# Kernel optimization log

Measured on AMD Instinct MI355X. Metric: run time of the kernel, lower is better.

The kernel has to match this reference:

```python
import jax, jax.numpy as jnp
import numpy as np

N = 20000   # nodes
E = 160000  # edges
C = 512     # input_size / channels
D = 16      # edge_size
H = 256     # hidden_size
EPS = 1e-5  # BatchNorm eps (eval mode, init running stats: mean=0, var=1)


def setup_inputs() -> dict:
    key = jax.random.key(0)
    ks = jax.random.split(key, 24)
    w = lambda k, shape: (jax.random.normal(k, shape, jnp.float32) * 0.02)
    inp = {
        "x": jax.random.normal(ks[0], (N, C), jnp.float32),
        "edge_index": jax.random.randint(ks[1], (2, E), 0, N, jnp.int32),
        "edge_attr": jax.random.normal(ks[2], (E, D), jnp.float32),
        "goal_feat": jax.random.normal(ks[3], (N, C), jnp.float32),
        # CGConv 1
        "Wf1": w(ks[4], (2 * C + D, C)), "bf1": jnp.zeros((C,), jnp.float32),
        "Ws1": w(ks[5], (2 * C + D, C)), "bs1": jnp.zeros((C,), jnp.float32),
        "g1": jnp.ones((C,), jnp.float32), "be1": jnp.zeros((C,), jnp.float32),
        # CGConv 2
        "Wf2": w(ks[6], (2 * C + D, C)), "bf2": jnp.zeros((C,), jnp.float32),
        "Ws2": w(ks[7], (2 * C + D, C)), "bs2": jnp.zeros((C,), jnp.float32),
        "g2": jnp.ones((C,), jnp.float32), "be2": jnp.zeros((C,), jnp.float32),
        # GCNConv 3, 4
        "W3": w(ks[8], (C, H)), "b3": jnp.zeros((H,), jnp.float32),
        "W4": w(ks[9], (H, H)), "b4": jnp.zeros((H,), jnp.float32),
        # distance MLP: Lin(H+C -> C), ReLU, Lin(C -> 1)
        "Wd1": w(ks[10], (H + C, C)), "bd1": jnp.zeros((C,), jnp.float32),
        "Wd2": w(ks[11], (C, 1)), "bd2": jnp.zeros((1,), jnp.float32),
    }
    return inp


def cg_conv(x, src, dst, edge_attr, Wf, bf, Ws, bs, gamma, beta):
    # PyG CGConv: z = x_i || x_j || e;  m = sigmoid(lin_f(z)) * softplus(lin_s(z))
    # aggr='add' at targets, BatchNorm (eval, init stats), residual.
    z = jnp.concatenate([x[dst], x[src], edge_attr], axis=-1)  # [E, 2C+D]
    m = jax.nn.sigmoid(z @ Wf + bf) * jax.nn.softplus(z @ Ws + bs)  # [E, C]
    agg = jax.ops.segment_sum(m, dst, num_segments=N)  # [N, C]
    agg = agg * (gamma / jnp.sqrt(1.0 + EPS)) + beta   # BN eval (mean=0, var=1)
    return agg + x


def gcn_conv(x, src, dst, W, b):
    # PyG GCNConv with add_self_loops=True, normalize=True
    h = x @ W  # [N, out]
    loop = jnp.arange(N, dtype=src.dtype)
    s = jnp.concatenate([src, loop])
    d = jnp.concatenate([dst, loop])
    deg = jax.ops.segment_sum(jnp.ones_like(d, jnp.float32), d, num_segments=N)
    dinv = jnp.where(deg > 0, jax.lax.rsqrt(jnp.maximum(deg, 1.0)), 0.0)
    norm = dinv[s] * dinv[d]  # [E+N]
    out = jax.ops.segment_sum(norm[:, None] * h[s], d, num_segments=N)
    return out + b


def reference(x, edge_index, edge_attr, goal_feat,
              Wf1, bf1, Ws1, bs1, g1, be1,
              Wf2, bf2, Ws2, bs2, g2, be2,
              W3, b3, W4, b4, Wd1, bd1, Wd2, bd2):
    src = edge_index[0]  # x_j (source)
    dst = edge_index[1]  # x_i (target)
    h = jax.nn.relu(cg_conv(x, src, dst, edge_attr, Wf1, bf1, Ws1, bs1, g1, be1))
    h = jax.nn.relu(cg_conv(h, src, dst, edge_attr, Wf2, bf2, Ws2, bs2, g2, be2))
    h = jax.nn.relu(gcn_conv(h, src, dst, W3, b3))
    h = jax.nn.relu(gcn_conv(h, src, dst, W4, b4))
    z = jnp.concatenate([h, goal_feat], axis=1)  # [N, H+C]
    pred_dist = jax.nn.relu(z @ Wd1 + bd1) @ Wd2 + bd2  # [N, 1]
    return pred_dist, h
```

## Files before the change

kernel.cpp:

```cpp
#include <hip/hip_runtime.h>
#include <stdint.h>

#define NNODES 20000
#define NEDGES 160000
#define NPAD   20096

typedef float f32x4 __attribute__((ext_vector_type(4)));
typedef float f32x2 __attribute__((ext_vector_type(2)));
typedef short s16x8 __attribute__((ext_vector_type(8)));
typedef unsigned int u32x4 __attribute__((ext_vector_type(4)));
typedef _Float16 h16x2 __attribute__((ext_vector_type(2)));

__device__ __forceinline__ float b2f(unsigned short b) {
    unsigned int u = ((unsigned int)b) << 16;
    return __builtin_bit_cast(float, u);
}
__device__ __forceinline__ unsigned short f2b(float f) {
    unsigned int u = __builtin_bit_cast(unsigned int, f);
    unsigned int r = (u + 0x7FFFu + ((u >> 16) & 1u)) >> 16;
    return (unsigned short)r;
}
__device__ __forceinline__ f32x2 unpack2(unsigned int u) {
    f32x2 r;
    r.x = __builtin_bit_cast(float, u << 16);
    r.y = __builtin_bit_cast(float, u & 0xFFFF0000u);
    return r;
}
__device__ __forceinline__ unsigned int packh2(float a, float b) {
    h16x2 h = { (_Float16)a, (_Float16)b };
    return __builtin_bit_cast(unsigned int, h);
}
__device__ __forceinline__ float dot2h(unsigned int a, unsigned int b, float c) {
#if __has_builtin(__builtin_amdgcn_fdot2)
    return __builtin_amdgcn_fdot2(__builtin_bit_cast(h16x2, a),
                                  __builtin_bit_cast(h16x2, b), c, false);
#else
    float d;
    asm("v_dot2_f32_f16 %0, %1, %2, %3" : "=v"(d) : "v"(a), "v"(b), "v"(c));
    return d;
#endif
}

__global__ __launch_bounds__(256) void gemm_bt_kernel(
    const unsigned short* __restrict__ A,
    const unsigned short* __restrict__ BT,
    float* __restrict__ Cf,
    unsigned short* __restrict__ Cb,
    int M, int N, int K,
    const float* __restrict__ bias)
{
    __shared__ unsigned short As[128 * 32];
    __shared__ unsigned short Bs[128 * 32];
    const int tid  = threadIdx.x;
    const int wid  = tid >> 6;
    const int lane = tid & 63;
    const int bm = blockIdx.x * 128;
    const int bn = blockIdx.y * 128;
    const int wm = (wid & 1) * 64;
    const int wn = (wid >> 1) * 64;

    f32x4 acc[4][4];
#pragma unroll
    for (int i = 0; i < 4; i++)
#pragma unroll
        for (int j = 0; j < 4; j++) acc[i][j] = {0.f, 0.f, 0.f, 0.f};

    for (int k0 = 0; k0 < K; k0 += 32) {
#pragma unroll
        for (int r = 0; r < 2; r++) {
            int flat = r * 256 + tid;
            int row  = flat >> 2;
            int part = flat & 3;
            const unsigned short* ga = A  + (size_t)(bm + row) * K + k0 + part * 8;
            const unsigned short* gb = BT + (size_t)(bn + row) * K + k0 + part * 8;
            __builtin_amdgcn_global_load_lds(
                (const __attribute__((address_space(1))) unsigned int*)ga,
                (__attribute__((address_space(3))) unsigned int*)&As[flat * 8], 16, 0, 0);
            __builtin_amdgcn_global_load_lds(
                (const __attribute__((address_space(1))) unsigned int*)gb,
                (__attribute__((address_space(3))) unsigned int*)&Bs[flat * 8], 16, 0, 0);
        }
        __syncthreads();

        const int kq = (lane >> 4) * 8;
        const int rl = lane & 15;
        s16x8 af[4], bfr[4];
#pragma unroll
        for (int mi = 0; mi < 4; mi++)
            af[mi] = *(const s16x8*)&As[(wm + mi * 16 + rl) * 32 + kq];
#pragma unroll
        for (int ni = 0; ni < 4; ni++)
            bfr[ni] = *(const s16x8*)&Bs[(wn + ni * 16 + rl) * 32 + kq];
#pragma unroll
        for (int mi = 0; mi < 4; mi++)
#pragma unroll
            for (int ni = 0; ni < 4; ni++)
                acc[mi][ni] = __builtin_amdgcn_mfma_f32_16x16x32_bf16(
                    af[mi], bfr[ni], acc[mi][ni], 0, 0, 0);
        __syncthreads();
    }

    const int cl = lane & 15;
    const int rq = (lane >> 4) * 4;
#pragma unroll
    for (int mi = 0; mi < 4; mi++)
#pragma unroll
        for (int ni = 0; ni < 4; ni++)
#pragma unroll
            for (int r = 0; r < 4; r++) {
                int row = bm + wm + mi * 16 + rq + r;
                int col = bn + wn + ni * 16 + cl;
                float v = acc[mi][ni][r];
                if (Cb) {
                    if (bias) v = fmaxf(v + bias[col], 0.f);
                    Cb[(size_t)row * N + col] = f2b(v);
                } else {
                    Cf[(size_t)row * N + col] = v;
                }
            }
}

__global__ void count_kernel(const int* __restrict__ ei, int* __restrict__ counts) {
    int e = blockIdx.x * blockDim.x + threadIdx.x;
    if (e < NEDGES) atomicAdd(&counts[ei[NEDGES + e]], 1);
}

__global__ __launch_bounds__(1024) void scan_kernel(const int* __restrict__ counts,
                                                    int* __restrict__ row_ptr)
{
    __shared__ int sdata[1024];
    const int t = threadIdx.x;
    int vals[20];
    const int base = t * 20;
    int lsum = 0;
#pragma unroll
    for (int j = 0; j < 20; j++) {
        int idx = base + j;
        int v = (idx < NNODES) ? counts[idx] : 0;
        vals[j] = v; lsum += v;
    }
    sdata[t] = lsum;
    __syncthreads();
    for (int off = 1; off < 1024; off <<= 1) {
        int v = (t >= off) ? sdata[t - off] : 0;
        __syncthreads();
        sdata[t] += v;
        __syncthreads();
    }
    int run = sdata[t] - lsum;
#pragma unroll
    for (int j = 0; j < 20; j++) {
        int idx = base + j;
        if (idx < NNODES) row_ptr[idx] = run;
        run += vals[j];
    }
    if (t == 1023) row_ptr[NNODES] = sdata[1023];
}

__global__ void fill_kernel(const int* __restrict__ ei,
                            const int* __restrict__ row_ptr,
                            int* __restrict__ cursor,
                            int2* __restrict__ csr)
{
    int e = blockIdx.x * blockDim.x + threadIdx.x;
    if (e >= NEDGES) return;
    int dst = ei[NEDGES + e];
    int p = row_ptr[dst] + atomicAdd(&cursor[dst], 1);
    csr[p] = make_int2(ei[e], e);
}

__global__ void dinv_kernel(const int* __restrict__ row_ptr, float* __restrict__ dinv) {
    int i = blockIdx.x * blockDim.x + threadIdx.x;
    if (i < NNODES) {
        int deg = row_ptr[i + 1] - row_ptr[i] + 1;
        dinv[i] = rsqrtf((float)deg);
    }
}

__global__ void pad_copy_kernel(const float* __restrict__ src,
                                unsigned short* __restrict__ dst,
                                int valid_rows, int cols, long total)
{
    long idx = (long)blockIdx.x * blockDim.x + threadIdx.x;
    if (idx >= total) return;
    int n = (int)(idx / cols);
    dst[idx] = (n < valid_rows) ? f2b(src[idx]) : (unsigned short)0;
}

__global__ void pack_cgw_kernel(const float* __restrict__ Wf,
                                const float* __restrict__ Ws,
                                unsigned short* __restrict__ out)
{
    int idx = blockIdx.x * blockDim.x + threadIdx.x;
    if (idx >= 2048 * 512) return;
    int j = idx >> 9;
    int k = idx & 511;
    int half = (j >= 1024);
    int jj = j & 1023;
    int c  = (jj >> 2) * 2 + (jj & 1);
    int fs = (jj >> 1) & 1;
    const float* W = fs ? Ws : Wf;
    float v = W[(size_t)(half ? 512 + k : k) * 512 + c];
    out[idx] = f2b(v);
}

__global__ void pack_t_kernel(const float* __restrict__ W,
                              unsigned short* __restrict__ WT,
                              int K, int Nout)
{
    long idx = (long)blockIdx.x * blockDim.x + threadIdx.x;
    if (idx >= (long)K * Nout) return;
    int j = (int)(idx / K);
    int k = (int)(idx % K);
    WT[idx] = f2b(W[(size_t)k * Nout + j]);
}

__global__ void pack_we_kernel(const float* __restrict__ Wf,
                               const float* __restrict__ Ws,
                               unsigned int* __restrict__ out)
{
    int idx = blockIdx.x * blockDim.x + threadIdx.x;
    if (idx >= 8192) return;
    int q  = idx & 3;
    int c2 = (idx >> 2) & 255;
    int k  = idx >> 10;
    const float* W = (q >> 1) ? Ws : Wf;
    int c = c2 * 2 + (q & 1);
    float v0 = W[(size_t)(1024 + 2 * k) * 512 + c];
    float v1 = W[(size_t)(1024 + 2 * k + 1) * 512 + c];
    out[idx] = packh2(v0, v1);
}

__global__ void pack_ea_kernel(const int2* __restrict__ csr,
                               const float* __restrict__ ea,
                               unsigned int* __restrict__ out)
{
    int idx = blockIdx.x * blockDim.x + threadIdx.x;
    if (idx >= NEDGES * 8) return;
    int i = idx >> 3;
    int j = idx & 7;
    int eid = csr[i].y;
    out[idx] = packh2(ea[(size_t)eid * 16 + 2 * j], ea[(size_t)eid * 16 + 2 * j + 1]);
}

#define CG_NPB 4
__global__ __launch_bounds__(256, 1) void cg_gather_kernel(
    const unsigned short* __restrict__ P,
    const int* __restrict__ row_ptr,
    const int2* __restrict__ csr,
    const u32x4* __restrict__ wE,
    const u32x4* __restrict__ eapk,
    const float* __restrict__ bfv,
    const float* __restrict__ bsv,
    const float* __restrict__ g,
    const float* __restrict__ be,
    const float* __restrict__ xresf,
    const unsigned short* __restrict__ xresb,
    unsigned short* __restrict__ hout)
{
    const int tid = threadIdx.x;
    const int c0  = tid * 2;
    const int nbase = blockIdx.x * CG_NPB;

    u32x4 w[8];
#pragma unroll
    for (int k = 0; k < 8; k++) w[k] = wE[k * 256 + tid];

    const f32x2 bfx = *(const f32x2*)&bfv[c0];
    const f32x2 bsx = *(const f32x2*)&bsv[c0];
    const f32x2 gv  = *(const f32x2*)&g[c0];
    const f32x2 bev = *(const f32x2*)&be[c0];
    const float rs = rsqrtf(1.f + 1e-5f);

    for (int n = nbase; n < nbase + CG_NPB; n++) {
        if (n >= NNODES) {
            *(unsigned int*)&hout[(size_t)n * 512 + c0] = 0;
            continue;
        }
        const unsigned short* Pd = P + (size_t)n * 2048;
        const uint2 qb = *(const uint2*)(Pd + c0 * 2);
        const f32x2 baseF = unpack2(qb.x) + bfx;
        const f32x2 baseS = unpack2(qb.y) + bsx;

        f32x2 acc = {0.f, 0.f};
        const int i0 = row_ptr[n], i1 = row_ptr[n + 1];

        auto do_edge = [&](int i) {
            const int sx = __builtin_amdgcn_readfirstlane(csr[i].x);
            u32x4 a0 = eapk[(size_t)i * 2];
            u32x4 a1 = eapk[(size_t)i * 2 + 1];
            uint2 q = *(const uint2*)(P + (size_t)sx * 2048 + 1024 + c0 * 2);
            float f0 = baseF.x, f1 = baseF.y, s0 = baseS.x, s1 = baseS.y;
#pragma unroll
            for (int k = 0; k < 4; k++) {
                f0 = dot2h(a0[k], w[k][0], f0);
                f1 = dot2h(a0[k], w[k][1], f1);
                s0 = dot2h(a0[k], w[k][2], s0);
                s1 = dot2h(a0[k], w[k][3], s1);
            }
#pragma unroll
            for (int k = 0; k < 4; k++) {
                f0 = dot2h(a1[k], w[4 + k][0], f0);
                f1 = dot2h(a1[k], w[4 + k][1], f1);
                s0 = dot2h(a1[k], w[4 + k][2], s0);
                s1 = dot2h(a1[k], w[4 + k][3], s1);
            }
            f32x2 pf = unpack2(q.x);
            f32x2 ps = unpack2(q.y);
            f0 += pf.x; f1 += pf.y; s0 += ps.x; s1 += ps.y;
            float sp0 = __logf(1.f + __expf(s0));
            float sp1 = __logf(1.f + __expf(s1));
            float sg0 = __builtin_amdgcn_rcpf(1.f + __expf(-f0));
            float sg1 = __builtin_amdgcn_rcpf(1.f + __expf(-f1));
            acc.x = fmaf(sp0, sg0, acc.x);
            acc.y = fmaf(sp1, sg1, acc.y);
        };

        int i = i0;
        for (; i + 1 < i1; i += 2) {
            do_edge(i);
            do_edge(i + 1);
        }
        if (i < i1) do_edge(i);

        f32x2 res;
        if (xresf) {
            res = *(const f32x2*)&xresf[(size_t)n * 512 + c0];
        } else {
            res = unpack2(*(const unsigned int*)&xresb[(size_t)n * 512 + c0]);
        }
        float v0 = fmaxf(acc.x * (gv.x * rs) + bev.x + res.x, 0.f);
        float v1 = fmaxf(acc.y * (gv.y * rs) + bev.y + res.y, 0.f);
        unsigned int packed = (unsigned int)f2b(v0) | ((unsigned int)f2b(v1) << 16);
        *(unsigned int*)&hout[(size_t)n * 512 + c0] = packed;
    }
}

__global__ __launch_bounds__(256) void gcn_gather_kernel(
    const unsigned short* __restrict__ pre,
    const int* __restrict__ row_ptr,
    const int2* __restrict__ csr,
    const float* __restrict__ dinv,
    const float* __restrict__ b,
    unsigned short* __restrict__ hout,
    float* __restrict__ doutf)
{
    const int tid = threadIdx.x;
    const int n = blockIdx.x * 2 + (tid >> 7);
    const int c = (tid & 127) * 2;
    if (n >= NNODES) {
        if (n < NPAD) *(unsigned int*)&hout[(size_t)n * 256 + c] = 0;
        return;
    }
    const float din = dinv[n];
    f32x2 acc = {0.f, 0.f};
    const int i0 = row_ptr[n], i1 = row_ptr[n + 1];
    if (i0 < i1) {
        int sx = __builtin_amdgcn_readfirstlane(csr[i0].x);
        float dv = dinv[sx];
        unsigned int pv = *(const unsigned int*)&pre[(size_t)sx * 256 + c];
        for (int i = i0; i < i1; i++) {
            float cdv = dv; unsigned int cpv = pv;
            if (i + 1 < i1) {
                int sx2 = __builtin_amdgcn_readfirstlane(csr[i + 1].x);
                dv = dinv[sx2];
                pv = *(const unsigned int*)&pre[(size_t)sx2 * 256 + c];
            }
            f32x2 p = unpack2(cpv);
            acc.x = fmaf(cdv, p.x, acc.x);
            acc.y = fmaf(cdv, p.y, acc.y);
        }
    }
    f32x2 self = unpack2(*(const unsigned int*)&pre[(size_t)n * 256 + c]);
    const f32x2 bv = *(const f32x2*)&b[c];
    float v0 = fmaxf(fmaf(acc.x, din, din * din * self.x) + bv.x, 0.f);
    float v1 = fmaxf(fmaf(acc.y, din, din * din * self.y) + bv.y, 0.f);
    *(unsigned int*)&hout[(size_t)n * 256 + c] =
        (unsigned int)f2b(v0) | ((unsigned int)f2b(v1) << 16);
    if (doutf) {
        f32x2 vv = {v0, v1};
        *(f32x2*)&doutf[(size_t)n * 256 + c] = vv;
    }
}

__global__ void build_zc_kernel(const unsigned short* __restrict__ h4,
                                const float* __restrict__ goal,
                                unsigned short* __restrict__ zc)
{
    long idx = (long)blockIdx.x * blockDim.x + threadIdx.x;
    if (idx >= (long)NPAD * 768) return;
    int n = (int)(idx / 768);
    int c = (int)(idx % 768);
    unsigned short v = 0;
    if (n < NNODES)
        v = (c < 256) ? h4[(size_t)n * 256 + c]
                      : f2b(goal[(size_t)n * 512 + (c - 256)]);
    zc[idx] = v;
}

__global__ __launch_bounds__(256) void final_dot_kernel(
    const unsigned short* __restrict__ t,
    const float* __restrict__ Wd2,
    const float* __restrict__ bd2,
    float* __restrict__ pred)
{
    const int lane = threadIdx.x & 63;
    const int wid  = threadIdx.x >> 6;
    float w[8];
#pragma unroll
    for (int i = 0; i < 8; i++) w[i] = Wd2[lane * 8 + i];
    const float bd = bd2[0];
    for (int n = blockIdx.x * 4 + wid; n < NNODES; n += gridDim.x * 4) {
        const unsigned short* tp = t + (size_t)n * 512 + lane * 8;
        float s = 0.f;
#pragma unroll
        for (int i = 0; i < 8; i++) s = fmaf(b2f(tp[i]), w[i], s);
#pragma unroll
        for (int off = 32; off; off >>= 1) s += __shfl_xor(s, off, 64);
        if (lane == 0) pred[n] = s + bd;
    }
}

extern "C" void kernel_launch(void* const* d_in, const int* in_sizes, int n_in,
                              void* d_out, int out_size, void* d_ws, size_t ws_size,
                              hipStream_t stream)
{
    (void)in_sizes; (void)n_in; (void)out_size; (void)ws_size;
    const float* x    = (const float*)d_in[0];
    const int*   ei   = (const int*)d_in[1];
    const float* ea   = (const float*)d_in[2];
    const float* goal = (const float*)d_in[3];
    const float* Wf1  = (const float*)d_in[4];
    const float* bf1  = (const float*)d_in[5];
    const float* Ws1  = (const float*)d_in[6];
    const float* bs1  = (const float*)d_in[7];
    const float* g1   = (const float*)d_in[8];
    const float* be1  = (const float*)d_in[9];
    const float* Wf2  = (const float*)d_in[10];
    const float* bf2  = (const float*)d_in[11];
    const float* Ws2  = (const float*)d_in[12];
    const float* bs2  = (const float*)d_in[13];
    const float* g2   = (const float*)d_in[14];
    const float* be2  = (const float*)d_in[15];
    const float* W3   = (const float*)d_in[16];
    const float* b3   = (const float*)d_in[17];
    const float* W4   = (const float*)d_in[18];
    const float* b4   = (const float*)d_in[19];
    const float* Wd1  = (const float*)d_in[20];
    const float* bd1  = (const float*)d_in[21];
    const float* Wd2  = (const float*)d_in[22];
    const float* bd2  = (const float*)d_in[23];
    float* outp = (float*)d_out;

    char* ws = (char*)d_ws;
    size_t off = 0;
    auto alloc = [&](size_t bytes) -> char* {
        char* p = ws + off;
        off += (bytes + 255) & ~(size_t)255;
        return p;
    };
    unsigned short* P     = (unsigned short*)alloc((size_t)NPAD * 2048 * 2);
    unsigned short* bufA  = (unsigned short*)alloc((size_t)NPAD * 512 * 2);
    unsigned short* bufB  = (unsigned short*)alloc((size_t)NPAD * 512 * 2);
    unsigned short* bufC  = (unsigned short*)alloc((size_t)NPAD * 512 * 2);
    unsigned short* wpack = (unsigned short*)alloc((size_t)2048 * 512 * 2);
    int*            counts  = (int*)alloc((size_t)NNODES * 4);
    int*            row_ptr = (int*)alloc((size_t)(NNODES + 1) * 4);
    int2*           csr     = (int2*)alloc((size_t)NEDGES * 8);
    float*          dinv    = (float*)alloc((size_t)NNODES * 4);
    unsigned int*   wEbuf   = (unsigned int*)alloc((size_t)8192 * 4);
    unsigned int*   eapk    = (unsigned int*)alloc((size_t)NEDGES * 8 * 4);

    unsigned short* xpad  = bufA;
    unsigned short* h1    = bufB;
    unsigned short* h2    = bufA;
    unsigned short* pre_b = bufB;
    unsigned short* h3    = bufC;
    unsigned short* h4    = bufA;
    unsigned short* zc    = P;
    unsigned short* tb    = P + (size_t)NPAD * 1024;

    const int B = 256;

    hipMemsetAsync(counts, 0, (size_t)NNODES * 4, stream);
    count_kernel<<<(NEDGES + B - 1) / B, B, 0, stream>>>(ei, counts);
    scan_kernel<<<1, 1024, 0, stream>>>(counts, row_ptr);
    hipMemsetAsync(counts, 0, (size_t)NNODES * 4, stream);
    fill_kernel<<<(NEDGES + B - 1) / B, B, 0, stream>>>(ei, row_ptr, counts, csr);
    dinv_kernel<<<(NNODES + B - 1) / B, B, 0, stream>>>(row_ptr, dinv);
    pack_ea_kernel<<<(NEDGES * 8 + B - 1) / B, B, 0, stream>>>(csr, ea, eapk);

    {
        long tot = (long)NPAD * 512;
        pad_copy_kernel<<<(unsigned)((tot + B - 1) / B), B, 0, stream>>>(x, xpad, NNODES, 512, tot);
    }

    dim3 gBig(NPAD / 128, 2048 / 128);

    pack_cgw_kernel<<<(2048 * 512 + B - 1) / B, B, 0, stream>>>(Wf1, Ws1, wpack);
    pack_we_kernel<<<(8192 + B - 1) / B, B, 0, stream>>>(Wf1, Ws1, wEbuf);
    gemm_bt_kernel<<<gBig, B, 0, stream>>>(xpad, wpack, nullptr, P, NPAD, 2048, 512, nullptr);
    cg_gather_kernel<<<NPAD / CG_NPB, B, 0, stream>>>(P, row_ptr, csr,
                                                      (const u32x4*)wEbuf, (const u32x4*)eapk,
                                                      bf1, bs1, g1, be1,
                                                      x, nullptr, h1);

    pack_cgw_kernel<<<(2048 * 512 + B - 1) / B, B, 0, stream>>>(Wf2, Ws2, wpack);
    gemm_bt_kernel<<<gBig, B, 0, stream>>>(h1, wpack, nullptr, P, NPAD, 2048, 512, nullptr);
    pack_we_kernel<<<(8192 + B - 1) / B, B, 0, stream>>>(Wf2, Ws2, wEbuf);
    cg_gather_kernel<<<NPAD / CG_NPB, B, 0, stream>>>(P, row_ptr, csr,
                                                      (const u32x4*)wEbuf, (const u32x4*)eapk,
                                                      bf2, bs2, g2, be2,
                                                      nullptr, h1, h2);

    pack_t_kernel<<<(256 * 512 + B - 1) / B, B, 0, stream>>>(W3, wpack, 512, 256);
    gemm_bt_kernel<<<dim3(NPAD / 128, 2), B, 0, stream>>>(h2, wpack, nullptr, pre_b, NPAD, 256, 512, nullptr);
    gcn_gather_kernel<<<NPAD / 2, B, 0, stream>>>(pre_b, row_ptr, csr, dinv, b3, h3, (float*)nullptr);

    pack_t_kernel<<<(256 * 256 + B - 1) / B, B, 0, stream>>>(W4, wpack, 256, 256);
    gemm_bt_kernel<<<dim3(NPAD / 128, 2), B, 0, stream>>>(h3, wpack, nullptr, pre_b, NPAD, 256, 256, nullptr);
    gcn_gather_kernel<<<NPAD / 2, B, 0, stream>>>(pre_b, row_ptr, csr, dinv, b4, h4, outp + NNODES);

    build_zc_kernel<<<(unsigned)(((long)NPAD * 768 + B - 1) / B), B, 0, stream>>>(h4, goal, zc);
    pack_t_kernel<<<(512 * 768 + B - 1) / B, B, 0, stream>>>(Wd1, wpack, 768, 512);
    gemm_bt_kernel<<<dim3(NPAD / 128, 4), B, 0, stream>>>(zc, wpack, nullptr, tb, NPAD, 512, 768, bd1);
    final_dot_kernel<<<512, B, 0, stream>>>(tb, Wd2, bd2, outp);
}
```

Measured before the change: 821.4 us.

## Software-pipeline edge gathers two deep and split CSR into separate src/eid arrays

Splits the interleaved CSR int2 array into separate source and edge-id arrays so the gather kernels read only the source indices they need. The CG and GCN gather loops are software-pipelined with two in-flight edge loads (A/B buffers), issuing the loads for edge i+2 while edge i is being computed, and the row bounds are made wave-uniform via readfirstlane. CG_NPB drops from 4 to 2 nodes per block, doubling the block count to improve load balance. The double buffering adds register pressure in the CG kernel, which is already launch-bounded to one block.

```diff
diff --git a/kernel.cpp b/kernel.cpp
--- a/kernel.cpp
+++ b/kernel.cpp
@@ -160,13 +160,15 @@
 __global__ void fill_kernel(const int* __restrict__ ei,
                             const int* __restrict__ row_ptr,
                             int* __restrict__ cursor,
-                            int2* __restrict__ csr)
+                            int* __restrict__ csr_src,
+                            int* __restrict__ csr_eid)
 {
     int e = blockIdx.x * blockDim.x + threadIdx.x;
     if (e >= NEDGES) return;
     int dst = ei[NEDGES + e];
     int p = row_ptr[dst] + atomicAdd(&cursor[dst], 1);
-    csr[p] = make_int2(ei[e], e);
+    csr_src[p] = ei[e];
+    csr_eid[p] = e;
 }
 
 __global__ void dinv_kernel(const int* __restrict__ row_ptr, float* __restrict__ dinv) {
@@ -231,7 +233,7 @@
     out[idx] = packh2(v0, v1);
 }
 
-__global__ void pack_ea_kernel(const int2* __restrict__ csr,
+__global__ void pack_ea_kernel(const int* __restrict__ csr_eid,
                                const float* __restrict__ ea,
                                unsigned int* __restrict__ out)
 {
@@ -239,15 +241,50 @@
     if (idx >= NEDGES * 8) return;
     int i = idx >> 3;
     int j = idx & 7;
-    int eid = csr[i].y;
+    int eid = csr_eid[i];
     out[idx] = packh2(ea[(size_t)eid * 16 + 2 * j], ea[(size_t)eid * 16 + 2 * j + 1]);
 }
 
-#define CG_NPB 4
+#define CG_NPB 2
+
+#define CG_LOADE(q_, a0_, a1_, idx) do {                                       \
+    int sx_ = __builtin_amdgcn_readfirstlane(csr_src[idx]);                    \
+    q_  = *(const uint2*)(P + (size_t)sx_ * 2048 + 1024 + c0 * 2);             \
+    a0_ = eapk[(size_t)(idx) * 2];                                             \
+    a1_ = eapk[(size_t)(idx) * 2 + 1];                                         \
+} while (0)
+
+#define CG_COMP(q_, a0_, a1_) do {                                             \
+    float f0 = baseF.x, f1 = baseF.y, s0 = baseS.x, s1 = baseS.y;              \
+    _Pragma("unroll")                                                          \
+    for (int k = 0; k < 4; k++) {                                              \
+        f0 = dot2h(a0_[k], w[k][0], f0);                                       \
+        f1 = dot2h(a0_[k], w[k][1], f1);                                       \
+        s0 = dot2h(a0_[k], w[k][2], s0);                                       \
+        s1 = dot2h(a0_[k], w[k][3], s1);                                       \
+    }                                                                          \
+    _Pragma("unroll")                                                          \
+    for (int k = 0; k < 4; k++) {                                              \
+        f0 = dot2h(a1_[k], w[4 + k][0], f0);                                   \
+        f1 = dot2h(a1_[k], w[4 + k][1], f1);                                   \
+        s0 = dot2h(a1_[k], w[4 + k][2], s0);                                   \
+        s1 = dot2h(a1_[k], w[4 + k][3], s1);                                   \
+    }                                                                          \
+    f32x2 pf = unpack2(q_.x);                                                  \
+    f32x2 ps = unpack2(q_.y);                                                  \
+    f0 += pf.x; f1 += pf.y; s0 += ps.x; s1 += ps.y;                            \
+    float sp0 = __logf(1.f + __expf(s0));                                      \
+    float sp1 = __logf(1.f + __expf(s1));                                      \
+    float sg0 = __builtin_amdgcn_rcpf(1.f + __expf(-f0));                      \
+    float sg1 = __builtin_amdgcn_rcpf(1.f + __expf(-f1));                      \
+    acc.x = fmaf(sp0, sg0, acc.x);                                             \
+    acc.y = fmaf(sp1, sg1, acc.y);                                             \
+} while (0)
+
 __global__ __launch_bounds__(256, 1) void cg_gather_kernel(
     const unsigned short* __restrict__ P,
     const int* __restrict__ row_ptr,
-    const int2* __restrict__ csr,
+    const int* __restrict__ csr_src,
     const u32x4* __restrict__ wE,
     const u32x4* __restrict__ eapk,
     const float* __restrict__ bfv,
@@ -283,45 +320,24 @@
         const f32x2 baseS = unpack2(qb.y) + bsx;
 
         f32x2 acc = {0.f, 0.f};
-        const int i0 = row_ptr[n], i1 = row_ptr[n + 1];
-
-        auto do_edge = [&](int i) {
-            const int sx = __builtin_amdgcn_readfirstlane(csr[i].x);
-            u32x4 a0 = eapk[(size_t)i * 2];
-            u32x4 a1 = eapk[(size_t)i * 2 + 1];
-            uint2 q = *(const uint2*)(P + (size_t)sx * 2048 + 1024 + c0 * 2);
-            float f0 = baseF.x, f1 = baseF.y, s0 = baseS.x, s1 = baseS.y;
-#pragma unroll
-            for (int k = 0; k < 4; k++) {
-                f0 = dot2h(a0[k], w[k][0], f0);
-                f1 = dot2h(a0[k], w[k][1], f1);
-                s0 = dot2h(a0[k], w[k][2], s0);
-                s1 = dot2h(a0[k], w[k][3], s1);
+        const int i0 = __builtin_amdgcn_readfirstlane(row_ptr[n]);
+        const int i1 = __builtin_amdgcn_readfirstlane(row_ptr[n + 1]);
+
+        if (i0 < i1) {
+            uint2 qA = {}, qB = {};
+            u32x4 aA0 = {}, aA1 = {}, aB0 = {}, aB1 = {};
+            CG_LOADE(qA, aA0, aA1, i0);
+            if (i0 + 1 < i1) CG_LOADE(qB, aB0, aB1, i0 + 1);
+            int i = i0;
+            while (i < i1) {
+                CG_COMP(qA, aA0, aA1);
+                if (i + 2 < i1) CG_LOADE(qA, aA0, aA1, i + 2);
+                if (++i >= i1) break;
+                CG_COMP(qB, aB0, aB1);
+                if (i + 2 < i1) CG_LOADE(qB, aB0, aB1, i + 2);
+                ++i;
             }
-#pragma unroll
-            for (int k = 0; k < 4; k++) {
-                f0 = dot2h(a1[k], w[4 + k][0], f0);
-                f1 = dot2h(a1[k], w[4 + k][1], f1);
-                s0 = dot2h(a1[k], w[4 + k][2], s0);
-                s1 = dot2h(a1[k], w[4 + k][3], s1);
-            }
-            f32x2 pf = unpack2(q.x);
-            f32x2 ps = unpack2(q.y);
-            f0 += pf.x; f1 += pf.y; s0 += ps.x; s1 += ps.y;
-            float sp0 = __logf(1.f + __expf(s0));
-            float sp1 = __logf(1.f + __expf(s1));
-            float sg0 = __builtin_amdgcn_rcpf(1.f + __expf(-f0));
-            float sg1 = __builtin_amdgcn_rcpf(1.f + __expf(-f1));
-            acc.x = fmaf(sp0, sg0, acc.x);
-            acc.y = fmaf(sp1, sg1, acc.y);
-        };
-
-        int i = i0;
-        for (; i + 1 < i1; i += 2) {
-            do_edge(i);
-            do_edge(i + 1);
-        }
-        if (i < i1) do_edge(i);
+        }
 
         f32x2 res;
         if (xresf) {
@@ -339,7 +355,7 @@
 __global__ __launch_bounds__(256) void gcn_gather_kernel(
     const unsigned short* __restrict__ pre,
     const int* __restrict__ row_ptr,
-    const int2* __restrict__ csr,
+    const int* __restrict__ csr_src,
     const float* __restrict__ dinv,
     const float* __restrict__ b,
     unsigned short* __restrict__ hout,
@@ -354,21 +370,45 @@
     }
     const float din = dinv[n];
     f32x2 acc = {0.f, 0.f};
-    const int i0 = row_ptr[n], i1 = row_ptr[n + 1];
+    const int i0 = __builtin_amdgcn_readfirstlane(row_ptr[n]);
+    const int i1 = __builtin_amdgcn_readfirstlane(row_ptr[n + 1]);
     if (i0 < i1) {
-        int sx = __builtin_amdgcn_readfirstlane(csr[i0].x);
-        float dv = dinv[sx];
-        unsigned int pv = *(const unsigned int*)&pre[(size_t)sx * 256 + c];
-        for (int i = i0; i < i1; i++) {
-            float cdv = dv; unsigned int cpv = pv;
-            if (i + 1 < i1) {
-                int sx2 = __builtin_amdgcn_readfirstlane(csr[i + 1].x);
-                dv = dinv[sx2];
-                pv = *(const unsigned int*)&pre[(size_t)sx2 * 256 + c];
+        float dvA = 0.f, dvB = 0.f;
+        unsigned int pvA = 0, pvB = 0;
+        {
+            int sx = __builtin_amdgcn_readfirstlane(csr_src[i0]);
+            dvA = dinv[sx];
+            pvA = *(const unsigned int*)&pre[(size_t)sx * 256 + c];
+        }
+        if (i0 + 1 < i1) {
+            int sx = __builtin_amdgcn_readfirstlane(csr_src[i0 + 1]);
+            dvB = dinv[sx];
+            pvB = *(const unsigned int*)&pre[(size_t)sx * 256 + c];
+        }
+        int i = i0;
+        while (i < i1) {
+            {
+                f32x2 p = unpack2(pvA);
+                acc.x = fmaf(dvA, p.x, acc.x);
+                acc.y = fmaf(dvA, p.y, acc.y);
             }
-            f32x2 p = unpack2(cpv);
-            acc.x = fmaf(cdv, p.x, acc.x);
-            acc.y = fmaf(cdv, p.y, acc.y);
+            if (i + 2 < i1) {
+                int sx = __builtin_amdgcn_readfirstlane(csr_src[i + 2]);
+                dvA = dinv[sx];
+                pvA = *(const unsigned int*)&pre[(size_t)sx * 256 + c];
+            }
+            if (++i >= i1) break;
+            {
+                f32x2 p = unpack2(pvB);
+                acc.x = fmaf(dvB, p.x, acc.x);
+                acc.y = fmaf(dvB, p.y, acc.y);
+            }
+            if (i + 2 < i1) {
+                int sx = __builtin_amdgcn_readfirstlane(csr_src[i + 2]);
+                dvB = dinv[sx];
+                pvB = *(const unsigned int*)&pre[(size_t)sx * 256 + c];
+            }
+            ++i;
         }
     }
     f32x2 self = unpack2(*(const unsigned int*)&pre[(size_t)n * 256 + c]);
@@ -466,7 +506,8 @@
     unsigned short* wpack = (unsigned short*)alloc((size_t)2048 * 512 * 2);
     int*            counts  = (int*)alloc((size_t)NNODES * 4);
     int*            row_ptr = (int*)alloc((size_t)(NNODES + 1) * 4);
-    int2*           csr     = (int2*)alloc((size_t)NEDGES * 8);
+    int*            csr_src = (int*)alloc((size_t)NEDGES * 4);
+    int*            csr_eid = (int*)alloc((size_t)NEDGES * 4);
     float*          dinv    = (float*)alloc((size_t)NNODES * 4);
     unsigned int*   wEbuf   = (unsigned int*)alloc((size_t)8192 * 4);
     unsigned int*   eapk    = (unsigned int*)alloc((size_t)NEDGES * 8 * 4);
@@ -486,9 +527,9 @@
     count_kernel<<<(NEDGES + B - 1) / B, B, 0, stream>>>(ei, counts);
     scan_kernel<<<1, 1024, 0, stream>>>(counts, row_ptr);
     hipMemsetAsync(counts, 0, (size_t)NNODES * 4, stream);
-    fill_kernel<<<(NEDGES + B - 1) / B, B, 0, stream>>>(ei, row_ptr, counts, csr);
+    fill_kernel<<<(NEDGES + B - 1) / B, B, 0, stream>>>(ei, row_ptr, counts, csr_src, csr_eid);
     dinv_kernel<<<(NNODES + B - 1) / B, B, 0, stream>>>(row_ptr, dinv);
-    pack_ea_kernel<<<(NEDGES * 8 + B - 1) / B, B, 0, stream>>>(csr, ea, eapk);
+    pack_ea_kernel<<<(NEDGES * 8 + B - 1) / B, B, 0, stream>>>(csr_eid, ea, eapk);
 
     {
         long tot = (long)NPAD * 512;
@@ -500,7 +541,7 @@
     pack_cgw_kernel<<<(2048 * 512 + B - 1) / B, B, 0, stream>>>(Wf1, Ws1, wpack);
     pack_we_kernel<<<(8192 + B - 1) / B, B, 0, stream>>>(Wf1, Ws1, wEbuf);
     gemm_bt_kernel<<<gBig, B, 0, stream>>>(xpad, wpack, nullptr, P, NPAD, 2048, 512, nullptr);
-    cg_gather_kernel<<<NPAD / CG_NPB, B, 0, stream>>>(P, row_ptr, csr,
+    cg_gather_kernel<<<NPAD / CG_NPB, B, 0, stream>>>(P, row_ptr, csr_src,
                                                       (const u32x4*)wEbuf, (const u32x4*)eapk,
                                                       bf1, bs1, g1, be1,
                                                       x, nullptr, h1);
@@ -508,18 +549,18 @@
     pack_cgw_kernel<<<(2048 * 512 + B - 1) / B, B, 0, stream>>>(Wf2, Ws2, wpack);
     gemm_bt_kernel<<<gBig, B, 0, stream>>>(h1, wpack, nullptr, P, NPAD, 2048, 512, nullptr);
     pack_we_kernel<<<(8192 + B - 1) / B, B, 0, stream>>>(Wf2, Ws2, wEbuf);
-    cg_gather_kernel<<<NPAD / CG_NPB, B, 0, stream>>>(P, row_ptr, csr,
+    cg_gather_kernel<<<NPAD / CG_NPB, B, 0, stream>>>(P, row_ptr, csr_src,
                                                       (const u32x4*)wEbuf, (const u32x4*)eapk,
                                                       bf2, bs2, g2, be2,
                                                       nullptr, h1, h2);
 
     pack_t_kernel<<<(256 * 512 + B - 1) / B, B, 0, stream>>>(W3, wpack, 512, 256);
     gemm_bt_kernel<<<dim3(NPAD / 128, 2), B, 0, stream>>>(h2, wpack, nullptr, pre_b, NPAD, 256, 512, nullptr);
-    gcn_gather_kernel<<<NPAD / 2, B, 0, stream>>>(pre_b, row_ptr, csr, dinv, b3, h3, (float*)nullptr);
+    gcn_gather_kernel<<<NPAD / 2, B, 0, stream>>>(pre_b, row_ptr, csr_src, dinv, b3, h3, (float*)nullptr);
 
     pack_t_kernel<<<(256 * 256 + B - 1) / B, B, 0, stream>>>(W4, wpack, 256, 256);
     gemm_bt_kernel<<<dim3(NPAD / 128, 2), B, 0, stream>>>(h3, wpack, nullptr, pre_b, NPAD, 256, 256, nullptr);
-    gcn_gather_kernel<<<NPAD / 2, B, 0, stream>>>(pre_b, row_ptr, csr, dinv, b4, h4, outp + NNODES);
+    gcn_gather_kernel<<<NPAD / 2, B, 0, stream>>>(pre_b, row_ptr, csr_src, dinv, b4, h4, outp + NNODES);
 
     build_zc_kernel<<<(unsigned)(((long)NPAD * 768 + B - 1) / B), B, 0, stream>>>(h4, goal, zc);
     pack_t_kernel<<<(512 * 768 + B - 1) / B, B, 0, stream>>>(Wd1, wpack, 768, 512);
```

Result: faster. 794.0 us (-3.3%).
